# Kernel optimization log

Measured on AMD Instinct MI355X. Metric: run time of the kernel, lower is better.

## Reference

```python
import jax, jax.numpy as jnp
import numpy as np

B, T, F = 128, 64, 2048
N, H, C = 1024, 1024, 22  # neurons, hidden_size, num_classes


def setup_inputs() -> dict:
    key = jax.random.key(0)
    ks = jax.random.split(key, 9)
    def w(k, shape, fan_in):
        return jax.random.normal(k, shape, dtype=jnp.float32) / np.sqrt(fan_in)
    return {
        "x": jax.random.normal(ks[0], (B, T, F), dtype=jnp.float32),
        "W1": w(ks[1], (N, F), F),
        "b1": jnp.zeros((N,), jnp.float32),
        "W_ih": w(ks[2], (4 * H, N), N),
        "b_ih": jnp.zeros((4 * H,), jnp.float32),
        "W_hh": w(ks[3], (4 * H, H), H),
        "b_hh": jnp.zeros((4 * H,), jnp.float32),
        "Wc": w(ks[4], (C, H), H),
        "bc": jnp.zeros((C,), jnp.float32),
    }


def reference(x, W1, b1, W_ih, b_ih, W_hh, b_hh, Wc, bc):
    b, t, _ = x.shape
    h0 = jnp.zeros((b, H), x.dtype)
    c0 = jnp.zeros((b, H), x.dtype)
    # Precompute the input-side projections for every step (batched GEMMs):
    z = jax.nn.relu(jnp.einsum("btf,nf->btn", x, W1) + b1)        # [B,T,N]
    xg = jnp.einsum("btn,gn->btg", z, W_ih) + b_ih                 # [B,T,4H]

    def step(carry, xg_t):
        h, c = carry
        gates = xg_t + h @ W_hh.T + b_hh                           # [B,4H]
        i, f, g, o = jnp.split(gates, 4, axis=-1)                  # torch LSTMCell gate order
        c = jax.nn.sigmoid(f) * c + jax.nn.sigmoid(i) * jnp.tanh(g)
        h = jax.nn.sigmoid(o) * jnp.tanh(c)
        return (h, c), h

    _, hs = jax.lax.scan(step, (h0, c0), jnp.swapaxes(xg, 0, 1))    # hs: [T,B,H]
    scores = jnp.einsum("tbh,ch->tbc", hs, Wc) + bc                # [T,B,C]
    scores = jnp.swapaxes(scores, 0, 1).reshape(-1, Wc.shape[0])    # [B*T, C]
    return scores
```

## Files before the change

kernel.cpp:

```cpp
#include <hip/hip_runtime.h>
#include <hip/hip_bf16.h>

typedef short bf16x8 __attribute__((ext_vector_type(8)));
typedef float f32x4 __attribute__((ext_vector_type(4)));

#define B_ 128
#define T_ 64
#define F_ 2048
#define N_ 1024
#define H_ 1024
#define C_ 22

__device__ __forceinline__ ushort f2bf(float f) {
    union { float f; unsigned u; } v; v.f = f;
    unsigned u = v.u;
    unsigned r = (u + 0x7FFFu + ((u >> 16) & 1u)) >> 16;
    return (ushort)r;
}
__device__ __forceinline__ float bf2f(ushort h) {
    union { unsigned u; float f; } v; v.u = ((unsigned)h) << 16;
    return v.f;
}

__global__ __launch_bounds__(256) void cvt_f32_bf16(const float* __restrict__ in,
                                                    ushort* __restrict__ out, int n4) {
    int i = blockIdx.x * blockDim.x + threadIdx.x;
    if (i < n4) {
        float4 v = ((const float4*)in)[i];
        ushort4 o;
        o.x = f2bf(v.x); o.y = f2bf(v.y); o.z = f2bf(v.z); o.w = f2bf(v.w);
        ((ushort4*)out)[i] = o;
    }
}

__global__ __launch_bounds__(256) void cvt_wc(const float* __restrict__ Wc,
                                              ushort* __restrict__ Wcb) {
    int i = blockIdx.x * 256 + threadIdx.x;
    int row = i >> 10;
    Wcb[i] = (row < C_) ? f2bf(Wc[i]) : (ushort)0;
}

__device__ __forceinline__ void gload16(const void* g, void* l) {
    __builtin_amdgcn_global_load_lds(
        (const __attribute__((address_space(1))) unsigned int*)g,
        (__attribute__((address_space(3))) unsigned int*)l, 16, 0, 0);
}

template<int K, bool RELU>
__global__ __launch_bounds__(256) void gemm_bt(const ushort* __restrict__ A,
                                               const ushort* __restrict__ Bm,
                                               const float* __restrict__ bias1,
                                               const float* __restrict__ bias2,
                                               ushort* __restrict__ C,
                                               int Nt, int Nn) {
    __shared__ ushort sA[128 * 32];
    __shared__ ushort sB[128 * 32];
    const int tid = threadIdx.x;
    const int lane = tid & 63, wv = tid >> 6;
    const int tm = blockIdx.x / Nt, tn = blockIdx.x % Nt;
    const int wm = wv >> 1, wn = wv & 1;

    const ushort* gA = A + (size_t)(tm * 128 + (tid >> 2)) * K + (tid & 3) * 8;
    const ushort* gB = Bm + (size_t)(tn * 128 + (tid >> 2)) * K + (tid & 3) * 8;
    char* lAb = (char*)sA + wv * 1024;
    char* lBb = (char*)sB + wv * 1024;

    f32x4 acc[4][4] = {};

    for (int kt = 0; kt < K / 32; kt++) {
        const ushort* a0 = gA + kt * 32;
        const ushort* b0 = gB + kt * 32;
        gload16(a0, lAb);
        gload16(a0 + 64 * K, lAb + 4096);
        gload16(b0, lBb);
        gload16(b0 + 64 * K, lBb + 4096);
        __syncthreads();

        bf16x8 af[4], bfv[4];
#pragma unroll
        for (int i = 0; i < 4; i++)
            af[i] = *(const bf16x8*)&sA[(wm * 64 + i * 16 + (lane & 15)) * 32 + (lane >> 4) * 8];
#pragma unroll
        for (int j = 0; j < 4; j++)
            bfv[j] = *(const bf16x8*)&sB[(wn * 64 + j * 16 + (lane & 15)) * 32 + (lane >> 4) * 8];
#pragma unroll
        for (int i = 0; i < 4; i++)
#pragma unroll
            for (int j = 0; j < 4; j++)
                acc[i][j] = __builtin_amdgcn_mfma_f32_16x16x32_bf16(af[i], bfv[j], acc[i][j], 0, 0, 0);
        __syncthreads();
    }

#pragma unroll
    for (int j = 0; j < 4; j++) {
        int n = tn * 128 + wn * 64 + j * 16 + (lane & 15);
        float bias = bias1[n] + (bias2 ? bias2[n] : 0.f);
#pragma unroll
        for (int i = 0; i < 4; i++) {
            int mbase = tm * 128 + wm * 64 + i * 16 + (lane >> 4) * 4;
#pragma unroll
            for (int r = 0; r < 4; r++) {
                float v = acc[i][j][r] + bias;
                if (RELU) v = v > 0.f ? v : 0.f;
                C[(size_t)(mbase + r) * Nn + n] = f2bf(v);
            }
        }
    }
}

__global__ __launch_bounds__(256, 1) void lstm_persist(ushort* __restrict__ hs,
                                                       const ushort* __restrict__ xg,
                                                       const ushort* __restrict__ Whh,
                                                       unsigned* __restrict__ cnt) {
    const int tid = threadIdx.x;
    const int lane = tid & 63;
    const int wv = tid >> 6;
    const int blk = (int)blockIdx.x;
    const int batch0 = (blk >> 6) * 32;
    const int hid0 = (blk & 63) * 16;
    const int bt = blk >> 6;

    bf16x8 breg[32];
    {
        const ushort* br = Whh + (size_t)(wv * H_ + hid0 + (lane & 15)) * H_ + ((lane >> 4) * 8);
#pragma unroll
        for (int ks = 0; ks < 32; ks++) breg[ks] = *(const bf16x8*)(br + ks * 32);
#pragma unroll
        for (int ks = 0; ks < 32; ks++) asm volatile("" : "+v"(breg[ks]));
    }

    __shared__ float lg[4][32][16];

    const int grow = tid >> 3;
    const int gjp = (tid & 7) * 2;
    float c0 = 0.f, c1 = 0.f;

    const int b = batch0 + grow;
    const int jj = hid0 + gjp;
    const ushort* xrow = xg + ((size_t)(b * T_) << 12) + jj;

    for (int t = 0; t < T_; t++) {
        const ushort* xr = xrow + ((size_t)t << 12);
        uint xi = *(const uint*)(xr);
        uint xf = *(const uint*)(xr + 1024);
        uint xgv = *(const uint*)(xr + 2048);
        uint xo = *(const uint*)(xr + 3072);

        const ushort* ar = hs + (size_t)t * (B_ * H_)
                         + (size_t)(batch0 + (lane & 15)) * H_ + ((lane >> 4) * 8);
        f32x4 acc0 = {}, acc1 = {};
#pragma unroll
        for (int ks = 0; ks < 32; ks++) {
            bf16x8 a0 = *(const bf16x8*)(ar + ks * 32);
            bf16x8 a1 = *(const bf16x8*)(ar + 16 * H_ + ks * 32);
            acc0 = __builtin_amdgcn_mfma_f32_16x16x32_bf16(a0, breg[ks], acc0, 0, 0, 0);
            acc1 = __builtin_amdgcn_mfma_f32_16x16x32_bf16(a1, breg[ks], acc1, 0, 0, 0);
        }
#pragma unroll
        for (int r = 0; r < 4; r++) {
            lg[wv][(lane >> 4) * 4 + r][lane & 15] = acc0[r];
            lg[wv][16 + (lane >> 4) * 4 + r][lane & 15] = acc1[r];
        }
        __syncthreads();

        {
            float pi0 = bf2f((ushort)(xi & 0xffff)) + lg[0][grow][gjp];
            float pi1 = bf2f((ushort)(xi >> 16)) + lg[0][grow][gjp + 1];
            float pf0 = bf2f((ushort)(xf & 0xffff)) + lg[1][grow][gjp];
            float pf1 = bf2f((ushort)(xf >> 16)) + lg[1][grow][gjp + 1];
            float pg0 = bf2f((ushort)(xgv & 0xffff)) + lg[2][grow][gjp];
            float pg1 = bf2f((ushort)(xgv >> 16)) + lg[2][grow][gjp + 1];
            float po0 = bf2f((ushort)(xo & 0xffff)) + lg[3][grow][gjp];
            float po1 = bf2f((ushort)(xo >> 16)) + lg[3][grow][gjp + 1];
            float si0 = 1.f / (1.f + expf(-pi0)), si1 = 1.f / (1.f + expf(-pi1));
            float sf0 = 1.f / (1.f + expf(-pf0)), sf1 = 1.f / (1.f + expf(-pf1));
            float tg0 = tanhf(pg0), tg1 = tanhf(pg1);
            float so0 = 1.f / (1.f + expf(-po0)), so1 = 1.f / (1.f + expf(-po1));
            c0 = sf0 * c0 + si0 * tg0;
            c1 = sf1 * c1 + si1 * tg1;
            uint hp = (uint)f2bf(so0 * tanhf(c0)) | ((uint)f2bf(so1 * tanhf(c1)) << 16);
            unsigned* hp32 = (unsigned*)(hs + (size_t)(t + 1) * (B_ * H_) + (size_t)b * H_ + jj);
            __hip_atomic_store(hp32, hp, __ATOMIC_RELAXED, __HIP_MEMORY_SCOPE_AGENT);
        }
        __syncthreads();

        if (t < T_ - 1) {
            unsigned* cp = cnt + ((size_t)(bt * T_ + t) << 4);
            if (tid == 0)
                atomicAdd(cp, 1u);
            if (wv == 0) {
                for (;;) {
                    unsigned v = __hip_atomic_load(cp, __ATOMIC_RELAXED,
                                                   __HIP_MEMORY_SCOPE_AGENT);
                    if (v >= 64u) break;
                    __builtin_amdgcn_s_sleep(1);
                }
            }
            __syncthreads();
        }
    }
}

__global__ __launch_bounds__(256) void scores_mfma(const ushort* __restrict__ hs,
                                                   const ushort* __restrict__ Wcb,
                                                   const float* __restrict__ bc,
                                                   float* __restrict__ out) {
    const int tid = threadIdx.x, lane = tid & 63, w = tid >> 6;
    const int r0 = blockIdx.x * 64 + w * 16;
    const int rr = r0 + (lane & 15);
    const int b = rr >> 6, t = rr & 63;
    const ushort* arow = hs + (size_t)(t + 1) * (B_ * H_) + (size_t)b * H_ + ((lane >> 4) * 8);
    const ushort* brow0 = Wcb + (size_t)(lane & 15) * H_ + ((lane >> 4) * 8);
    const ushort* brow1 = brow0 + 16 * H_;

    f32x4 acc0 = {}, acc1 = {};
#pragma unroll
    for (int ks = 0; ks < 32; ks++) {
        bf16x8 a  = *(const bf16x8*)(arow + ks * 32);
        bf16x8 p0 = *(const bf16x8*)(brow0 + ks * 32);
        bf16x8 p1 = *(const bf16x8*)(brow1 + ks * 32);
        acc0 = __builtin_amdgcn_mfma_f32_16x16x32_bf16(a, p0, acc0, 0, 0, 0);
        acc1 = __builtin_amdgcn_mfma_f32_16x16x32_bf16(a, p1, acc1, 0, 0, 0);
    }
#pragma unroll
    for (int nf = 0; nf < 2; nf++) {
        int c = nf * 16 + (lane & 15);
        if (c < C_) {
            float bias = bc[c];
            f32x4 acc = nf ? acc1 : acc0;
#pragma unroll
            for (int r = 0; r < 4; r++) {
                int row = r0 + (lane >> 4) * 4 + r;
                out[(size_t)row * C_ + c] = acc[r] + bias;
            }
        }
    }
}

extern "C" void kernel_launch(void* const* d_in, const int* in_sizes, int n_in,
                              void* d_out, int out_size, void* d_ws, size_t ws_size,
                              hipStream_t stream) {
    const float* x = (const float*)d_in[0];
    const float* W1 = (const float*)d_in[1];
    const float* b1 = (const float*)d_in[2];
    const float* W_ih = (const float*)d_in[3];
    const float* b_ih = (const float*)d_in[4];
    const float* W_hh = (const float*)d_in[5];
    const float* b_hh = (const float*)d_in[6];
    const float* Wc = (const float*)d_in[7];
    const float* bc = (const float*)d_in[8];
    float* out = (float*)d_out;

    char* ws = (char*)d_ws;
    ushort* Xb   = (ushort*)(ws);
    ushort* W1b  = (ushort*)(ws + 33554432);
    ushort* Wihb = (ushort*)(ws + 37748736);
    ushort* Whhb = (ushort*)(ws + 46137344);
    ushort* z    = (ushort*)(ws + 54525952);
    ushort* xg   = (ushort*)(ws + 71303168);
    ushort* hs   = (ushort*)(ws + 138412032);
    ushort* Wcb  = (ushort*)(ws + 155451392);
    unsigned* cnt = (unsigned*)(ws + 155516928);

    hipMemsetAsync(hs, 0, (size_t)B_ * H_ * sizeof(ushort), stream);
    hipMemsetAsync(cnt, 0, 32768, stream);

    cvt_f32_bf16<<<16384, 256, 0, stream>>>(x, Xb, 4194304);
    cvt_f32_bf16<<<2048, 256, 0, stream>>>(W1, W1b, 524288);
    cvt_f32_bf16<<<4096, 256, 0, stream>>>(W_ih, Wihb, 1048576);
    cvt_f32_bf16<<<4096, 256, 0, stream>>>(W_hh, Whhb, 1048576);
    cvt_wc<<<128, 256, 0, stream>>>(Wc, Wcb);

    gemm_bt<2048, true><<<512, 256, 0, stream>>>(Xb, W1b, b1, nullptr, z, 8, 1024);
    gemm_bt<1024, false><<<2048, 256, 0, stream>>>(z, Wihb, b_ih, b_hh, xg, 32, 4096);

    lstm_persist<<<256, 256, 0, stream>>>(hs, xg, Whhb, cnt);

    scores_mfma<<<128, 256, 0, stream>>>(hs, Wcb, bc, out);
}
```

Baseline: 821.3 us.

## Stage W_hh in swizzled LDS and prefetch xg before the step barrier

The persistent LSTM kernel now copies its slice of W_hh into a 128 KB swizzled LDS buffer with async global-to-LDS loads, instead of pinning it in 32 bf16x8 registers per lane. Each step issues the next xg tile load into LDS before waiting on the inter-block step counter, so that load can overlap the barrier spin. This frees VGPRs and hides xg latency. In exchange every MFMA step now adds LDS reads of W_hh, and the large LDS footprint depends on the gload16 helper and the swizzle being correct.

```diff
diff --git a/kernel.cpp b/kernel.cpp
--- a/kernel.cpp
+++ b/kernel.cpp
@@ -112,6 +112,10 @@
                                                        const ushort* __restrict__ xg,
                                                        const ushort* __restrict__ Whh,
                                                        unsigned* __restrict__ cnt) {
+    __shared__ ushort wlds[65536];
+    __shared__ ushort xlds[2048];
+    __shared__ float lg[4][32][16];
+
     const int tid = threadIdx.x;
     const int lane = tid & 63;
     const int wv = tid >> 6;
@@ -120,16 +124,21 @@
     const int hid0 = (blk & 63) * 16;
     const int bt = blk >> 6;
 
-    bf16x8 breg[32];
     {
-        const ushort* br = Whh + (size_t)(wv * H_ + hid0 + (lane & 15)) * H_ + ((lane >> 4) * 8);
-#pragma unroll
-        for (int ks = 0; ks < 32; ks++) breg[ks] = *(const bf16x8*)(br + ks * 32);
-#pragma unroll
-        for (int ks = 0; ks < 32; ks++) asm volatile("" : "+v"(breg[ks]));
-    }
-
-    __shared__ float lg[4][32][16];
+        const char* wsrc = (const char*)(Whh + (size_t)(wv * H_ + hid0) * H_);
+        char* wdst = (char*)wlds + wv * 32768;
+        for (int i = 0; i < 32; i++) {
+            int o = i * 1024 + lane * 16;
+            int osw = o ^ (((o >> 11) & 7) << 4);
+            gload16(wsrc + osw, wdst + i * 1024);
+        }
+    }
+    __syncthreads();
+
+    const int r15 = lane & 15, qq = lane >> 4;
+    const int swz = (r15 & 7) << 4;
+    const char* wb = (const char*)wlds + wv * 32768;
+    const int apre = r15 * 2048 + qq * 16;
 
     const int grow = tid >> 3;
     const int gjp = (tid & 7) * 2;
@@ -137,33 +146,53 @@
 
     const int b = batch0 + grow;
     const int jj = hid0 + gjp;
-    const ushort* xrow = xg + ((size_t)(b * T_) << 12) + jj;
+
+    const int cc = wv * 64 + lane;
+    const int srow = cc >> 3, sgate = (cc >> 1) & 3, shalf = cc & 1;
+    const ushort* xsrc0 = xg + ((size_t)((batch0 + srow) * T_) << 12)
+                        + sgate * H_ + hid0 + shalf * 8;
+    const char* xrb = (const char*)xlds + (grow * 8 + (gjp >> 3)) * 16 + (gjp & 7) * 2;
 
     for (int t = 0; t < T_; t++) {
-        const ushort* xr = xrow + ((size_t)t << 12);
-        uint xi = *(const uint*)(xr);
-        uint xf = *(const uint*)(xr + 1024);
-        uint xgv = *(const uint*)(xr + 2048);
-        uint xo = *(const uint*)(xr + 3072);
+        gload16(xsrc0 + ((size_t)t << 12), (char*)xlds + wv * 1024);
+
+        if (t > 0) {
+            unsigned* cp = cnt + ((size_t)(bt * T_ + (t - 1)) << 4);
+            if (tid == 0) atomicAdd(cp, 1u);
+            if (wv == 0) {
+                for (;;) {
+                    unsigned v = __hip_atomic_load(cp, __ATOMIC_RELAXED,
+                                                   __HIP_MEMORY_SCOPE_AGENT);
+                    if (v >= 64u) break;
+                    __builtin_amdgcn_s_sleep(1);
+                }
+            }
+            __syncthreads();
+        }
 
         const ushort* ar = hs + (size_t)t * (B_ * H_)
-                         + (size_t)(batch0 + (lane & 15)) * H_ + ((lane >> 4) * 8);
+                         + (size_t)(batch0 + r15) * H_ + (qq * 8);
         f32x4 acc0 = {}, acc1 = {};
 #pragma unroll
         for (int ks = 0; ks < 32; ks++) {
             bf16x8 a0 = *(const bf16x8*)(ar + ks * 32);
             bf16x8 a1 = *(const bf16x8*)(ar + 16 * H_ + ks * 32);
-            acc0 = __builtin_amdgcn_mfma_f32_16x16x32_bf16(a0, breg[ks], acc0, 0, 0, 0);
-            acc1 = __builtin_amdgcn_mfma_f32_16x16x32_bf16(a1, breg[ks], acc1, 0, 0, 0);
+            bf16x8 bfr = *(const bf16x8*)(wb + ((apre + ks * 64) ^ swz));
+            acc0 = __builtin_amdgcn_mfma_f32_16x16x32_bf16(a0, bfr, acc0, 0, 0, 0);
+            acc1 = __builtin_amdgcn_mfma_f32_16x16x32_bf16(a1, bfr, acc1, 0, 0, 0);
         }
 #pragma unroll
         for (int r = 0; r < 4; r++) {
-            lg[wv][(lane >> 4) * 4 + r][lane & 15] = acc0[r];
-            lg[wv][16 + (lane >> 4) * 4 + r][lane & 15] = acc1[r];
+            lg[wv][qq * 4 + r][r15] = acc0[r];
+            lg[wv][16 + qq * 4 + r][r15] = acc1[r];
         }
         __syncthreads();
 
         {
+            uint xi  = *(const uint*)(xrb);
+            uint xf  = *(const uint*)(xrb + 32);
+            uint xgv = *(const uint*)(xrb + 64);
+            uint xo  = *(const uint*)(xrb + 96);
             float pi0 = bf2f((ushort)(xi & 0xffff)) + lg[0][grow][gjp];
             float pi1 = bf2f((ushort)(xi >> 16)) + lg[0][grow][gjp + 1];
             float pf0 = bf2f((ushort)(xf & 0xffff)) + lg[1][grow][gjp];
@@ -183,21 +212,6 @@
             __hip_atomic_store(hp32, hp, __ATOMIC_RELAXED, __HIP_MEMORY_SCOPE_AGENT);
         }
         __syncthreads();
-
-        if (t < T_ - 1) {
-            unsigned* cp = cnt + ((size_t)(bt * T_ + t) << 4);
-            if (tid == 0)
-                atomicAdd(cp, 1u);
-            if (wv == 0) {
-                for (;;) {
-                    unsigned v = __hip_atomic_load(cp, __ATOMIC_RELAXED,
-                                                   __HIP_MEMORY_SCOPE_AGENT);
-                    if (v >= 64u) break;
-                    __builtin_amdgcn_s_sleep(1);
-                }
-            }
-            __syncthreads();
-        }
     }
 }
 
```

New measurement: 838.9 us (median of 3 runs). 1.02x slower.
